# Kernel tuning notes

Hardware: AMD Instinct MI355X
Metric: run time of the kernel (lower is better)

Reference implementation:

```python
import jax, jax.numpy as jnp
import numpy as np

B, L, P, D = 512, 32, 256, 2


def hungarian(cost):
    """Min-cost assignment on an [n,n] numpy cost matrix (rows=pred, cols=target).
    Returns col[row]: target index assigned to each pred row (same as scipy
    linear_sum_assignment col_ind). Jonker-Volgenant style augmenting path."""
    n = cost.shape[0]
    INF = 1e18
    u = np.zeros(n + 1)
    v = np.zeros(n + 1)
    p = np.zeros(n + 1, dtype=np.int64)
    way = np.zeros(n + 1, dtype=np.int64)
    for i in range(1, n + 1):
        p[0] = i
        j0 = 0
        minv = np.full(n + 1, INF)
        used = np.zeros(n + 1, dtype=bool)
        while True:
            used[j0] = True
            i0 = p[j0]
            free = ~used[1:]
            cur = cost[i0 - 1, :] - u[i0] - v[1:]
            upd = free & (cur < minv[1:])
            m1 = minv[1:]
            m1[upd] = cur[upd]
            w1 = way[1:]
            w1[upd] = j0
            mfree = np.where(free, m1, INF)
            j1 = int(np.argmin(mfree)) + 1
            delta = mfree[j1 - 1]
            u[p[used]] += delta
            v[used] -= delta
            m1[free] -= delta
            j0 = j1
            if p[j0] == 0:
                break
        while j0:
            j1 = way[j0]
            p[j0] = p[j1]
            j0 = j1
    col = np.zeros(n, dtype=np.int64)
    for j in range(1, n + 1):
        col[p[j] - 1] = j - 1
    return col


def match_targets_np(pred_flat, tgt_flat, n_lines):
    """pred_flat/tgt_flat: np [B, L, P*D]; n_lines: np int [B].
    Replicates match_lines_sequence: Hungarian on pairwise squared L2 over the
    first n valid lines; unmatched rows stay zero (they are masked in the loss)."""
    out = np.zeros_like(pred_flat)
    for b in range(pred_flat.shape[0]):
        n = int(n_lines[b])
        if n == 1:
            out[b] = tgt_flat[b]
            continue
        pr = pred_flat[b, :n]
        tg = tgt_flat[b, :n]
        cost = ((pr[:, None, :] - tg[None, :, :]) ** 2).sum(-1)  # [pred, target]
        col = hungarian(cost)
        out[b, :n] = tgt_flat[b][col]
    return out


def setup_inputs() -> dict:
    key = jax.random.key(0)
    ks = jax.random.split(key, 5)
    point_pos_pred = jax.random.normal(ks[0], (B, L, P, D), jnp.float32)
    target_pos = jax.random.normal(ks[1], (B, L, P, D), jnp.float32)
    # probabilities in (0,1), bounded away from 0 so -log is finite
    line_prob_pred = jax.random.uniform(ks[2], (B, L, 2), jnp.float32) * 0.9 + 0.05
    n_lines = jax.random.randint(ks[3], (B,), 1, L + 1)
    line_masks = (jnp.arange(L)[None, :] < n_lines[:, None]).astype(jnp.float32)
    clf_line = jax.random.randint(ks[4], (B, L), 0, 2).astype(jnp.int32)
    point_masks = (line_masks[:, :, None] * jnp.ones((1, 1, P), jnp.float32))
    return {
        "point_pos_pred": point_pos_pred,
        "line_prob_pred": line_prob_pred,
        "target_pos": target_pos,
        "line_masks": line_masks,
        "clf_line": clf_line,
        "point_masks": point_masks,
    }


def reference(point_pos_pred, line_prob_pred, target_pos, line_masks, clf_line, point_masks):
    # --- Hungarian matching (host-side, non-differentiable, as in the original) ---
    pp = np.asarray(point_pos_pred).reshape(B, L, P * D)
    tp = np.asarray(target_pos).reshape(B, L, P * D)
    n_lines = np.asarray(line_masks).sum(axis=1).astype(np.int64)
    matched = jnp.asarray(match_targets_np(pp, tp, n_lines)).reshape(B, L, P, D)
    # --- masked MSE over (point, dim) ---
    sq = jnp.sum((point_pos_pred - matched) ** 2, axis=-1) * point_masks  # [B,L,P]
    mask_mse = jnp.sum(sq) / jnp.sum(point_masks)
    # --- masked NLL on line existence probabilities ---
    neg_log = -jnp.log(line_prob_pred).reshape(-1, 2)        # [B*L, 2]
    picked = jnp.take_along_axis(neg_log, clf_line.reshape(-1, 1), axis=1)
    clf_loss = jnp.sum(picked * line_masks.reshape(-1, 1)) / jnp.sum(line_masks)
    return (mask_mse, clf_loss)
```

## Files before the change

kernel.cpp:

```cpp
#include <hip/hip_runtime.h>
#include <cstdint>
#include <cstddef>

#define NB 512
#define NL 32
#define KD 512
#define KSLAB 256
#define PASS 128

__device__ __forceinline__ int swz128(int row, int ch) {
  int csw = (ch & ~15) | ((ch ^ (row >> 1)) & 15);
  return row * PASS + csw * 4;
}

__global__ __launch_bounds__(256, 2)
void cost_kernel(const float* __restrict__ pred, const float* __restrict__ tgt,
                 float* __restrict__ cost_part) {
  __shared__ float smem[8192];
  const int bid = blockIdx.x;
  const int b  = bid >> 1;
  const int ks = (bid & 1) * KSLAB;
  const int tid = threadIdx.x;
  float* predH = smem;
  float* tgtH  = smem + 4096;

  const int w = tid >> 6, l = tid & 63;
  const int ti = l >> 3, tj = l & 7;
  float acc[4][4];
#pragma unroll
  for (int a = 0; a < 4; ++a)
#pragma unroll
    for (int c2 = 0; c2 < 4; ++c2) acc[a][c2] = 0.f;

  for (int hp = 0; hp < 2; ++hp) {
    __syncthreads();
    const size_t base = (size_t)b * (NL * KD) + ks + hp * PASS;
#pragma unroll
    for (int it = 0; it < 4; ++it) {
      int chunk = tid + it * 256;
      int row = chunk >> 5, ch = chunk & 31;
      const float4 pv = *reinterpret_cast<const float4*>(pred + base + (size_t)row * KD + ch * 4);
      const float4 tv = *reinterpret_cast<const float4*>(tgt  + base + (size_t)row * KD + ch * 4);
      int off = swz128(row, ch);
      *reinterpret_cast<float4*>(predH + off) = pv;
      *reinterpret_cast<float4*>(tgtH  + off) = tv;
    }
    __syncthreads();
#pragma unroll
    for (int c0 = 0; c0 < 8; ++c0) {
      const int c = (w << 3) + c0;
      float4 pr[4], tg[4];
#pragma unroll
      for (int r = 0; r < 4; ++r) {
        pr[r] = *reinterpret_cast<const float4*>(predH + swz128(4 * ti + r, c));
        tg[r] = *reinterpret_cast<const float4*>(tgtH  + swz128(4 * tj + r, c));
      }
#pragma unroll
      for (int a = 0; a < 4; ++a)
#pragma unroll
        for (int c2 = 0; c2 < 4; ++c2) {
          float d;
          d = pr[a].x - tg[c2].x; acc[a][c2] += d * d;
          d = pr[a].y - tg[c2].y; acc[a][c2] += d * d;
          d = pr[a].z - tg[c2].z; acc[a][c2] += d * d;
          d = pr[a].w - tg[c2].w; acc[a][c2] += d * d;
        }
    }
  }
  __syncthreads();
#pragma unroll
  for (int a = 0; a < 4; ++a)
#pragma unroll
    for (int c2 = 0; c2 < 4; ++c2)
      smem[w * 1024 + (ti & 3) + 4 * tj + 32 * a + 128 * c2 + 512 * (ti >> 2)] = acc[a][c2];
  __syncthreads();
  const int ti2 = tid >> 5, a2 = (tid >> 3) & 3, tj2 = tid & 7;
  float ov[4];
#pragma unroll
  for (int k = 0; k < 4; ++k) {
    int ad = (ti2 & 3) + 4 * tj2 + 32 * a2 + 128 * k + 512 * (ti2 >> 2);
    ov[k] = (smem[ad] + smem[ad + 1024]) + (smem[ad + 2048] + smem[ad + 3072]);
  }
  float4 o4 = make_float4(ov[0], ov[1], ov[2], ov[3]);
  *reinterpret_cast<float4*>(cost_part + (size_t)bid * 1024 + tid * 4) = o4;
}

__device__ __forceinline__ float readlane_f(float x, int lane) {
  return __int_as_float(__builtin_amdgcn_readlane(__float_as_int(x), lane));
}
__device__ __forceinline__ int readlane_i(int x, int lane) {
  return __builtin_amdgcn_readlane(x, lane);
}

template<int CTRL, int RM>
__device__ __forceinline__ float dppmin(float x) {
  int m = __builtin_amdgcn_update_dpp(__float_as_int(x), __float_as_int(x), CTRL, RM, 0xf, false);
  return fminf(x, __int_as_float(m));
}
__device__ __forceinline__ float wave_min32_bcast(float x) {
  x = dppmin<0xB1, 0xf>(x);
  x = dppmin<0x4E, 0xf>(x);
  x = dppmin<0x124, 0xf>(x);
  x = dppmin<0x128, 0xf>(x);
  x = dppmin<0x142, 0xa>(x);
  return readlane_f(x, 31);
}

__global__ __launch_bounds__(64)
void hung_kernel(const float* __restrict__ cost_part,
                 const float* __restrict__ prob,
                 const float* __restrict__ lmask,
                 const int* __restrict__ clf,
                 float* __restrict__ part) {
  __shared__ float cs[1024];
  const int b = blockIdx.x;
  const int lane = threadIdx.x;

  {
    const float4* c0p = reinterpret_cast<const float4*>(cost_part + (size_t)(2 * b) * 1024);
    const float4* c1p = reinterpret_cast<const float4*>(cost_part + (size_t)(2 * b + 1) * 1024);
    float4* cs4 = reinterpret_cast<float4*>(cs);
#pragma unroll
    for (int k = 0; k < 4; ++k) {
      int i = lane + 64 * k;
      float4 x = c0p[i], y = c1p[i];
      cs4[i] = make_float4(x.x + y.x, x.y + y.y, x.z + y.z, x.w + y.w);
    }
  }

  float lm = (lane < 32) ? lmask[b * 32 + lane] : 0.f;
  const int n = __popcll(__ballot(lm > 0.5f));
  float clfpart = 0.f;
  if (lane < 32 && lm > 0.5f) {
    int cc = clf[b * 32 + lane];
    clfpart = -logf(prob[(size_t)(b * 32 + lane) * 2 + cc]);
  }
  __syncthreads();

  const float FINF = 1e30f;
  const bool activecol = (lane < n);
  const int cl = lane & 31;

  float u_r = 0.f, v_j = 0.f;
  int p_j = -1;

  for (int ri = 0; ri < n; ++ri) {
    int i0 = ri;
    bool usedc = false;
    bool usedr = (lane == ri);
    float rowv = cs[i0 * 32 + cl];
    while (true) {
      float key = rowv - v_j;
      bool act = activecol && !usedc;
      float m = act ? key : FINF;
      float u0 = readlane_f(u_r, i0);
      float mn = wave_min32_bcast(m);
      uint64_t tie = __ballot(m == mn);
      int j1 = __ffsll((unsigned long long)tie) - 1;
      int pj1 = readlane_i(p_j, j1);
      int i0n = pj1 < 0 ? 0 : pj1;
      float rowv_n = cs[i0n * 32 + cl];
      float delta = mn - u0;
      if (usedr) u_r += delta;
      if (usedc) v_j -= delta;
      if (pj1 < 0) {
        if (lane == j1) p_j = ri;
        break;
      }
      usedc = usedc || (lane == j1);
      i0 = pj1;
      usedr = usedr || (lane == i0);
      rowv = rowv_n;
    }
  }

  int pj = p_j < 0 ? 0 : p_j;
  float a = activecol ? cs[pj * 32 + cl] : 0.f;
#pragma unroll
  for (int off = 32; off; off >>= 1) {
    a += __shfl_xor(a, off);
    clfpart += __shfl_xor(clfpart, off);
  }
  if (lane == 0) {
    part[b * 3 + 0] = a;
    part[b * 3 + 1] = clfpart;
    part[b * 3 + 2] = (float)n;
  }
}

__global__ void finalize_kernel(const float* __restrict__ part, float* __restrict__ out) {
  const int lane = threadIdx.x;
  double cs = 0.0, ls = 0.0, ns = 0.0;
  for (int i = lane; i < NB; i += 64) {
    cs += (double)part[i * 3 + 0];
    ls += (double)part[i * 3 + 1];
    ns += (double)part[i * 3 + 2];
  }
#pragma unroll
  for (int off = 32; off; off >>= 1) {
    cs += __shfl_xor(cs, off);
    ls += __shfl_xor(ls, off);
    ns += __shfl_xor(ns, off);
  }
  if (lane == 0) {
    out[0] = (float)(cs / (ns * 256.0));
    out[1] = (float)(ls / ns);
  }
}

extern "C" void kernel_launch(void* const* d_in, const int* in_sizes, int n_in,
                              void* d_out, int out_size, void* d_ws, size_t ws_size,
                              hipStream_t stream) {
  const float* pred = (const float*)d_in[0];
  const float* prob = (const float*)d_in[1];
  const float* tgt  = (const float*)d_in[2];
  const float* lm   = (const float*)d_in[3];
  const int*   clf  = (const int*)d_in[4];

  float* cost_part = (float*)d_ws;
  float* part = cost_part + (size_t)1024 * 1024;

  cost_kernel<<<NB * 2, 256, 0, stream>>>(pred, tgt, cost_part);
  hung_kernel<<<NB, 64, 0, stream>>>(cost_part, prob, lm, clf, part);
  finalize_kernel<<<1, 64, 0, stream>>>(part, (float*)d_out);
}
```

Before: 61.45 us.

## Fuse cost, Hungarian, and finalize kernels via atomic ticket last-block pattern

Merges the three launches into one kernel. Each batch's second-finishing cost block picks up the Hungarian matching for that batch, using a per-batch atomic ticket, and the globally last block performs the final reduction. This removes two kernel launch gaps and lets matching for early batches overlap with cost computation for others. In exchange it adds a memset launch, atomics and threadfences, and the winner block runs the serial Hungarian with only one wave while holding a 256-thread block's resources.

```diff
diff --git a/kernel.cpp b/kernel.cpp
--- a/kernel.cpp
+++ b/kernel.cpp
@@ -13,9 +13,38 @@
   return row * PASS + csw * 4;
 }
 
+__device__ __forceinline__ float readlane_f(float x, int lane) {
+  return __int_as_float(__builtin_amdgcn_readlane(__float_as_int(x), lane));
+}
+__device__ __forceinline__ int readlane_i(int x, int lane) {
+  return __builtin_amdgcn_readlane(x, lane);
+}
+
+template<int CTRL, int RM>
+__device__ __forceinline__ float dppmin(float x) {
+  int m = __builtin_amdgcn_update_dpp(__float_as_int(x), __float_as_int(x), CTRL, RM, 0xf, false);
+  return fminf(x, __int_as_float(m));
+}
+__device__ __forceinline__ float wave_min32_bcast(float x) {
+  x = dppmin<0xB1, 0xf>(x);
+  x = dppmin<0x4E, 0xf>(x);
+  x = dppmin<0x124, 0xf>(x);
+  x = dppmin<0x128, 0xf>(x);
+  x = dppmin<0x142, 0xa>(x);
+  return readlane_f(x, 31);
+}
+
 __global__ __launch_bounds__(256, 2)
-void cost_kernel(const float* __restrict__ pred, const float* __restrict__ tgt,
-                 float* __restrict__ cost_part) {
+void fused_kernel(const float* __restrict__ pred,
+                  const float* __restrict__ prob,
+                  const float* __restrict__ tgt,
+                  const float* __restrict__ lmask,
+                  const int* __restrict__ clf,
+                  float* __restrict__ cost_part,
+                  unsigned int* __restrict__ bticket,
+                  unsigned int* __restrict__ gticket,
+                  float* __restrict__ part,
+                  float* __restrict__ out) {
   __shared__ float smem[8192];
   const int bid = blockIdx.x;
   const int b  = bid >> 1;
@@ -81,41 +110,22 @@
     int ad = (ti2 & 3) + 4 * tj2 + 32 * a2 + 128 * k + 512 * (ti2 >> 2);
     ov[k] = (smem[ad] + smem[ad + 1024]) + (smem[ad + 2048] + smem[ad + 3072]);
   }
-  float4 o4 = make_float4(ov[0], ov[1], ov[2], ov[3]);
-  *reinterpret_cast<float4*>(cost_part + (size_t)bid * 1024 + tid * 4) = o4;
-}
-
-__device__ __forceinline__ float readlane_f(float x, int lane) {
-  return __int_as_float(__builtin_amdgcn_readlane(__float_as_int(x), lane));
-}
-__device__ __forceinline__ int readlane_i(int x, int lane) {
-  return __builtin_amdgcn_readlane(x, lane);
-}
-
-template<int CTRL, int RM>
-__device__ __forceinline__ float dppmin(float x) {
-  int m = __builtin_amdgcn_update_dpp(__float_as_int(x), __float_as_int(x), CTRL, RM, 0xf, false);
-  return fminf(x, __int_as_float(m));
-}
-__device__ __forceinline__ float wave_min32_bcast(float x) {
-  x = dppmin<0xB1, 0xf>(x);
-  x = dppmin<0x4E, 0xf>(x);
-  x = dppmin<0x124, 0xf>(x);
-  x = dppmin<0x128, 0xf>(x);
-  x = dppmin<0x142, 0xa>(x);
-  return readlane_f(x, 31);
-}
-
-__global__ __launch_bounds__(64)
-void hung_kernel(const float* __restrict__ cost_part,
-                 const float* __restrict__ prob,
-                 const float* __restrict__ lmask,
-                 const int* __restrict__ clf,
-                 float* __restrict__ part) {
-  __shared__ float cs[1024];
-  const int b = blockIdx.x;
-  const int lane = threadIdx.x;
-
+  *reinterpret_cast<float4*>(cost_part + (size_t)bid * 1024 + tid * 4) =
+      make_float4(ov[0], ov[1], ov[2], ov[3]);
+
+  volatile int* winflag = (int*)(smem + 1024);
+  __threadfence();
+  if (tid == 0) {
+    unsigned int t = atomicAdd(&bticket[b], 1u);
+    *winflag = (t == 1u);
+  }
+  __syncthreads();
+  if (!*winflag) return;
+  if (tid >= 64) return;
+  __threadfence();
+
+  const int lane = tid;
+  float* cs = smem;
   {
     const float4* c0p = reinterpret_cast<const float4*>(cost_part + (size_t)(2 * b) * 1024);
     const float4* c1p = reinterpret_cast<const float4*>(cost_part + (size_t)(2 * b + 1) * 1024);
@@ -135,7 +145,7 @@
     int cc = clf[b * 32 + lane];
     clfpart = -logf(prob[(size_t)(b * 32 + lane) * 2 + cc]);
   }
-  __syncthreads();
+  asm volatile("s_waitcnt lgkmcnt(0)" ::: "memory");
 
   const float FINF = 1e30f;
   const bool activecol = (lane < n);
@@ -186,25 +196,30 @@
     part[b * 3 + 1] = clfpart;
     part[b * 3 + 2] = (float)n;
   }
-}
-
-__global__ void finalize_kernel(const float* __restrict__ part, float* __restrict__ out) {
-  const int lane = threadIdx.x;
-  double cs = 0.0, ls = 0.0, ns = 0.0;
-  for (int i = lane; i < NB; i += 64) {
-    cs += (double)part[i * 3 + 0];
-    ls += (double)part[i * 3 + 1];
-    ns += (double)part[i * 3 + 2];
-  }
-#pragma unroll
-  for (int off = 32; off; off >>= 1) {
-    cs += __shfl_xor(cs, off);
-    ls += __shfl_xor(ls, off);
-    ns += __shfl_xor(ns, off);
-  }
-  if (lane == 0) {
-    out[0] = (float)(cs / (ns * 256.0));
-    out[1] = (float)(ls / ns);
+
+  __threadfence();
+  unsigned int t = 0;
+  if (lane == 0) t = atomicAdd(gticket, 1u);
+  t = (unsigned int)__shfl((int)t, 0);
+  if (t == NB - 1u) {
+    __threadfence();
+    volatile const float* vp = part;
+    double csum = 0.0, lsum = 0.0, nsum = 0.0;
+    for (int i = lane; i < NB; i += 64) {
+      csum += (double)vp[i * 3 + 0];
+      lsum += (double)vp[i * 3 + 1];
+      nsum += (double)vp[i * 3 + 2];
+    }
+#pragma unroll
+    for (int off = 32; off; off >>= 1) {
+      csum += __shfl_xor(csum, off);
+      lsum += __shfl_xor(lsum, off);
+      nsum += __shfl_xor(nsum, off);
+    }
+    if (lane == 0) {
+      out[0] = (float)(csum / (nsum * 256.0));
+      out[1] = (float)(lsum / nsum);
+    }
   }
 }
 
@@ -218,9 +233,11 @@
   const int*   clf  = (const int*)d_in[4];
 
   float* cost_part = (float*)d_ws;
-  float* part = cost_part + (size_t)1024 * 1024;
-
-  cost_kernel<<<NB * 2, 256, 0, stream>>>(pred, tgt, cost_part);
-  hung_kernel<<<NB, 64, 0, stream>>>(cost_part, prob, lm, clf, part);
-  finalize_kernel<<<1, 64, 0, stream>>>(part, (float*)d_out);
-}
+  unsigned int* bticket = (unsigned int*)(cost_part + (size_t)1024 * 1024);
+  unsigned int* gticket = bticket + NB;
+  float* part = (float*)(gticket + 1);
+
+  hipMemsetAsync(bticket, 0, (NB + 1) * sizeof(unsigned int), stream);
+  fused_kernel<<<NB * 2, 256, 0, stream>>>(pred, prob, tgt, lm, clf, cost_part,
+                                           bticket, gticket, part, (float*)d_out);
+}
```

After: 201.3 us. 3.28x slower.
